# Optimization experiments

Measured on AMD Instinct MI355X. Metric: run time of the kernel, lower is better.

The kernel has to match this reference:

```python
import jax, jax.numpy as jnp
import numpy as np

GROUP_SIZE = 128
IN_FEATURES = 8192
OUT_FEATURES = 28672
TOKENS = 32


def _dequantize(qweight, qzeros, scales):
    """ExLlama q4 dequant.
    qweight: (K//8, N) int32, 8 int4 values per word packed along k.
    qzeros:  (G, N//8) int32, 8 int4 zeros per word packed along n.
    scales:  (G, N) fp16.  g = k // GROUP_SIZE; w = s * (q - (z + 1)).
    """
    shifts = jnp.arange(8, dtype=jnp.int32) * 4
    K = qweight.shape[0] * 8
    N = qweight.shape[1]
    G = qzeros.shape[0]
    # unpack weights along k: (K//8, 8, N) -> (K, N)
    q = (qweight[:, None, :] >> shifts[None, :, None]) & 15
    q = q.reshape(K, N)
    # unpack zeros along n: (G, N//8, 8) -> (G, N)
    z = (qzeros[:, :, None] >> shifts[None, None, :]) & 15
    z = z.reshape(G, N)
    # group-wise dequant: reshape k into (G, GROUP_SIZE)
    qg = q.reshape(G, GROUP_SIZE, N).astype(jnp.float16)
    zf = (z + 1).astype(jnp.float16)[:, None, :]          # ExLlama stores zero-1
    w = (qg - zf) * scales[:, None, :]                    # (G, GS, N) fp16
    return w.reshape(K, N)


def setup_inputs() -> dict:
    key = jax.random.key(0)
    k1, k2, k3, k4, k5 = jax.random.split(key, 5)
    x = jax.random.normal(k1, (TOKENS, IN_FEATURES), dtype=jnp.float16)
    qweight = jax.random.randint(k2, (IN_FEATURES // 8, OUT_FEATURES),
                                 minval=-(2**31), maxval=2**31 - 1, dtype=jnp.int32)
    qzeros = jax.random.randint(k3, (IN_FEATURES // GROUP_SIZE, OUT_FEATURES // 8),
                                minval=-(2**31), maxval=2**31 - 1, dtype=jnp.int32)
    scales = (jax.random.uniform(k4, (IN_FEATURES // GROUP_SIZE, OUT_FEATURES),
                                 dtype=jnp.float32) * 0.01 + 0.001).astype(jnp.float16)
    bias = jax.random.normal(k5, (OUT_FEATURES,), dtype=jnp.float16)
    return {"x": x, "qweight": qweight, "qzeros": qzeros,
            "scales": scales, "bias": bias}


def reference(x, qweight, qzeros, scales, bias):
    w = _dequantize(qweight, qzeros, scales)              # (K, N) fp16
    out = jnp.matmul(x.astype(jnp.float16), w)            # (T, N)
    return out + bias
```

## Files before the change

### kernel.cpp

```cpp
#include <hip/hip_runtime.h>

#define T_TOK   32
#define KDIM    8192
#define NDIM    28672
#define NGRP    64
#define NZWORDS 3584
#define NSEG    16
#define SEGK    (KDIM / NSEG)
#define GPS     (NGRP / NSEG)
#define XROW    (SEGK + 8)

typedef _Float16 half8  __attribute__((ext_vector_type(8)));
typedef _Float16 half2v __attribute__((ext_vector_type(2)));
typedef float    f32x4  __attribute__((ext_vector_type(4)));
typedef unsigned uint4v __attribute__((ext_vector_type(4)));

template<bool ATOMIC>
__global__ __launch_bounds__(256)
void exllama_gemm_deep(const int*   __restrict__ qweight,
                       const int*   __restrict__ qzeros,
                       const float* __restrict__ scales,
                       const float* __restrict__ x,
                       const float* __restrict__ bias,
                       float*       __restrict__ ws,
                       float*       __restrict__ out)
{
    __shared__ alignas(16) _Float16 xs[T_TOK * XROW];

    const int tid  = threadIdx.x;
    const int lane = tid & 63;
    const int wav  = tid >> 6;
    const int quad = lane >> 4;
    const int l16  = lane & 15;
    const int seg  = blockIdx.y;
    const int n0   = blockIdx.x * 256 + wav * 64;

    int nc[4];
    #pragma unroll
    for (int j = 0; j < 4; ++j) nc[j] = n0 + j * 16 + l16;

    const int g0 = seg * GPS;

    unsigned qw[GPS][16];
    half2v   sp[GPS][4], cp[GPS][4];
    #pragma unroll
    for (int g = 0; g < GPS; ++g) {
        const size_t rb = (size_t)((g0 + g) * 16 + quad) * NDIM;
        #pragma unroll
        for (int c = 0; c < 4; ++c)
            #pragma unroll
            for (int j = 0; j < 4; ++j)
                qw[g][c * 4 + j] = (unsigned)qweight[rb + (size_t)(c * 4) * NDIM + nc[j]];
    }
    #pragma unroll
    for (int g = 0; g < GPS; ++g) {
        #pragma unroll
        for (int j = 0; j < 4; ++j) {
            float s  = scales[(size_t)(g0 + g) * NDIM + nc[j]];
            int   zw = qzeros[(size_t)(g0 + g) * NZWORDS + (nc[j] >> 3)];
            int   z  = (zw >> ((nc[j] & 7) * 4)) & 15;
            _Float16 sh = (_Float16)s;
            _Float16 ch = (_Float16)(float)(-(1025 + z));
            sp[g][j] = (half2v){sh, sh};
            cp[g][j] = (half2v){ch, ch};
        }
    }

    {
        const int kseg0 = seg * SEGK;
        #pragma unroll
        for (int it = 0; it < (T_TOK * SEGK) / (256 * 8); ++it) {
            const int e  = it * 2048 + tid * 8;
            const int t  = e >> 9;
            const int kl = e & (SEGK - 1);
            const float* xp = x + (size_t)t * KDIM + kseg0 + kl;
            f32x4 lo = *(const f32x4*)xp;
            f32x4 hi = *(const f32x4*)(xp + 4);
            uint4v u;
            #pragma unroll
            for (int j = 0; j < 4; ++j)
                u[j] = __builtin_bit_cast(unsigned,
                          __builtin_amdgcn_cvt_pkrtz(lo[j], hi[j]));
            *(uint4v*)(xs + t * XROW + kl) = u;
        }
    }
    __syncthreads();

    f32x4 acc[4][2];
    #pragma unroll
    for (int j = 0; j < 4; ++j)
        #pragma unroll
        for (int m = 0; m < 2; ++m)
            acc[j][m] = (f32x4){0.f, 0.f, 0.f, 0.f};

    #pragma unroll
    for (int g = 0; g < GPS; ++g) {
        #pragma unroll
        for (int c = 0; c < 4; ++c) {
            const int kloc = g * 128 + c * 32 + quad * 8;
            half8 a0 = *(const half8*)(xs + l16 * XROW + kloc);
            half8 a1 = *(const half8*)(xs + (l16 + 16) * XROW + kloc);
            #pragma unroll
            for (int j = 0; j < 4; ++j) {
                const unsigned w = qw[g][c * 4 + j];
                uint4v bu;
                #pragma unroll
                for (int i = 0; i < 4; ++i) {
                    unsigned t = ((w >> (4 * i)) & 0x000F000Fu) | 0x64006400u;
                    half2v th = __builtin_bit_cast(half2v, t);
                    half2v r  = (th + cp[g][j]) * sp[g][j];
                    bu[i] = __builtin_bit_cast(unsigned, r);
                }
                half8 bf = __builtin_bit_cast(half8, bu);
                acc[j][0] = __builtin_amdgcn_mfma_f32_16x16x32_f16(a0, bf, acc[j][0], 0, 0, 0);
                acc[j][1] = __builtin_amdgcn_mfma_f32_16x16x32_f16(a1, bf, acc[j][1], 0, 0, 0);
            }
        }
    }

    if (ATOMIC) {
        #pragma unroll
        for (int j = 0; j < 4; ++j) {
            const int n  = n0 + j * 16 + l16;
            const float bb = bias[n] * (1.0f / NSEG);
            #pragma unroll
            for (int m = 0; m < 2; ++m)
                #pragma unroll
                for (int r = 0; r < 4; ++r) {
                    const int t = m * 16 + quad * 4 + r;
                    unsafeAtomicAdd(out + (size_t)t * NDIM + n, acc[j][m][r] + bb);
                }
        }
    } else {
        float* wsp = ws + (size_t)seg * (T_TOK * NDIM);
        #pragma unroll
        for (int j = 0; j < 4; ++j) {
            const int n = n0 + j * 16 + l16;
            #pragma unroll
            for (int m = 0; m < 2; ++m)
                #pragma unroll
                for (int r = 0; r < 4; ++r) {
                    const int t = m * 16 + quad * 4 + r;
                    wsp[(size_t)t * NDIM + n] = acc[j][m][r];
                }
        }
    }
}

__global__ __launch_bounds__(256)
void reduce_bias(const float* __restrict__ ws,
                 const float* __restrict__ bias,
                 float*       __restrict__ out)
{
    const int e = (blockIdx.x * 256 + threadIdx.x) * 4;
    const int n = e % NDIM;
    f32x4 sum = (f32x4){0.f, 0.f, 0.f, 0.f};
    #pragma unroll
    for (int s = 0; s < NSEG; ++s)
        sum += *(const f32x4*)(ws + (size_t)s * (T_TOK * NDIM) + e);
    f32x4 bb = *(const f32x4*)(bias + n);
    *(f32x4*)(out + e) = sum + bb;
}

extern "C" void kernel_launch(void* const* d_in, const int* in_sizes, int n_in,
                              void* d_out, int out_size, void* d_ws, size_t ws_size,
                              hipStream_t stream)
{
    const float* x  = (const float*)d_in[0];
    const int* qweight = (const int*)d_in[1];
    const int* qzeros  = (const int*)d_in[2];
    const float* sc = (const float*)d_in[3];
    const float* bs = (const float*)d_in[4];
    float* out      = (float*)d_out;

    const size_t need = (size_t)NSEG * T_TOK * NDIM * sizeof(float);
    if (ws_size >= need) {
        exllama_gemm_deep<false><<<dim3(NDIM / 256, NSEG), 256, 0, stream>>>(
            qweight, qzeros, sc, x, bs, (float*)d_ws, out);
        reduce_bias<<<(T_TOK * NDIM) / (256 * 4), 256, 0, stream>>>(
            (const float*)d_ws, bs, out);
    } else {
        exllama_gemm_deep<true><<<dim3(NDIM / 256, NSEG), 256, 0, stream>>>(
            qweight, qzeros, sc, x, bs, nullptr, out);
    }
}
```

Baseline: 200.8 us.

## Replace split-K with full-K blocks using double-buffered software pipeline

```diff
diff --git a/kernel.cpp b/kernel.cpp
--- a/kernel.cpp
+++ b/kernel.cpp
@@ -3,163 +3,139 @@
 #define T_TOK   32
 #define KDIM    8192
 #define NDIM    28672
-#define NGRP    64
-#define NZWORDS 3584
-#define NSEG    16
-#define SEGK    (KDIM / NSEG)
-#define GPS     (NGRP / NSEG)
-#define XROW    (SEGK + 8)
+#define NZW     3584
+#define PHK     256
+#define NPH     (KDIM / PHK)
+#define GPP     (PHK / 128)
+#define XROW    (PHK + 8)
+#define XIT     ((T_TOK * PHK) / (256 * 8))
 
 typedef _Float16 half8  __attribute__((ext_vector_type(8)));
 typedef _Float16 half2v __attribute__((ext_vector_type(2)));
 typedef float    f32x4  __attribute__((ext_vector_type(4)));
 typedef unsigned uint4v __attribute__((ext_vector_type(4)));
 
-template<bool ATOMIC>
 __global__ __launch_bounds__(256)
-void exllama_gemm_deep(const int*   __restrict__ qweight,
-                       const int*   __restrict__ qzeros,
-                       const float* __restrict__ scales,
-                       const float* __restrict__ x,
-                       const float* __restrict__ bias,
-                       float*       __restrict__ ws,
-                       float*       __restrict__ out)
+void exllama_gemm_fullk(const int*   __restrict__ qweight,
+                        const int*   __restrict__ qzeros,
+                        const float* __restrict__ scales,
+                        const float* __restrict__ x,
+                        const float* __restrict__ bias,
+                        float*       __restrict__ out)
 {
-    __shared__ alignas(16) _Float16 xs[T_TOK * XROW];
+    __shared__ alignas(16) _Float16 xs[2][T_TOK * XROW];
 
     const int tid  = threadIdx.x;
     const int lane = tid & 63;
     const int wav  = tid >> 6;
     const int quad = lane >> 4;
     const int l16  = lane & 15;
-    const int seg  = blockIdx.y;
-    const int n0   = blockIdx.x * 256 + wav * 64;
+    const int n    = blockIdx.x * 64 + wav * 16 + l16;
 
-    int nc[4];
+    const float* xbase[XIT];
+    int          lofs[XIT];
     #pragma unroll
-    for (int j = 0; j < 4; ++j) nc[j] = n0 + j * 16 + l16;
-
-    const int g0 = seg * GPS;
-
-    unsigned qw[GPS][16];
-    half2v   sp[GPS][4], cp[GPS][4];
-    #pragma unroll
-    for (int g = 0; g < GPS; ++g) {
-        const size_t rb = (size_t)((g0 + g) * 16 + quad) * NDIM;
-        #pragma unroll
-        for (int c = 0; c < 4; ++c)
-            #pragma unroll
-            for (int j = 0; j < 4; ++j)
-                qw[g][c * 4 + j] = (unsigned)qweight[rb + (size_t)(c * 4) * NDIM + nc[j]];
-    }
-    #pragma unroll
-    for (int g = 0; g < GPS; ++g) {
-        #pragma unroll
-        for (int j = 0; j < 4; ++j) {
-            float s  = scales[(size_t)(g0 + g) * NDIM + nc[j]];
-            int   zw = qzeros[(size_t)(g0 + g) * NZWORDS + (nc[j] >> 3)];
-            int   z  = (zw >> ((nc[j] & 7) * 4)) & 15;
-            _Float16 sh = (_Float16)s;
-            _Float16 ch = (_Float16)(float)(-(1025 + z));
-            sp[g][j] = (half2v){sh, sh};
-            cp[g][j] = (half2v){ch, ch};
-        }
+    for (int it = 0; it < XIT; ++it) {
+        const int e  = it * 2048 + tid * 8;
+        const int t  = e >> 8;
+        const int kl = e & (PHK - 1);
+        xbase[it] = x + (size_t)t * KDIM + kl;
+        lofs[it]  = t * XROW + kl;
     }
 
-    {
-        const int kseg0 = seg * SEGK;
+    f32x4 xlo[XIT], xhi[XIT];
+    auto LOADX = [&](int p) {
         #pragma unroll
-        for (int it = 0; it < (T_TOK * SEGK) / (256 * 8); ++it) {
-            const int e  = it * 2048 + tid * 8;
-            const int t  = e >> 9;
-            const int kl = e & (SEGK - 1);
-            const float* xp = x + (size_t)t * KDIM + kseg0 + kl;
-            f32x4 lo = *(const f32x4*)xp;
-            f32x4 hi = *(const f32x4*)(xp + 4);
+        for (int it = 0; it < XIT; ++it) {
+            const float* xp = xbase[it] + p * PHK;
+            xlo[it] = *(const f32x4*)xp;
+            xhi[it] = *(const f32x4*)(xp + 4);
+        }
+    };
+    auto CVTW = [&](_Float16* buf) {
+        #pragma unroll
+        for (int it = 0; it < XIT; ++it) {
             uint4v u;
             #pragma unroll
             for (int j = 0; j < 4; ++j)
                 u[j] = __builtin_bit_cast(unsigned,
-                          __builtin_amdgcn_cvt_pkrtz(lo[j], hi[j]));
-            *(uint4v*)(xs + t * XROW + kl) = u;
+                          __builtin_amdgcn_cvt_pkrtz(xlo[it][j], xhi[it][j]));
+            *(uint4v*)(buf + lofs[it]) = u;
         }
-    }
-    __syncthreads();
+    };
+    auto LOADQ = [&](unsigned* qw, half2v* sp, half2v* cp, int p) {
+        #pragma unroll
+        for (int g = 0; g < GPP; ++g) {
+            const size_t rb = (size_t)(p * (PHK / 8) + g * 16 + quad) * NDIM + n;
+            #pragma unroll
+            for (int c = 0; c < 4; ++c)
+                qw[g * 4 + c] = (unsigned)qweight[rb + (size_t)(c * 4) * NDIM];
+            const float s  = scales[(size_t)(p * GPP + g) * NDIM + n];
+            const int   zw = qzeros[(size_t)(p * GPP + g) * NZW + (n >> 3)];
+            const int   z  = (zw >> ((n & 7) * 4)) & 15;
+            const _Float16 sh = (_Float16)s;
+            const _Float16 ch = (_Float16)(float)(-(1025 + z));
+            sp[g] = (half2v){sh, sh};
+            cp[g] = (half2v){ch, ch};
+        }
+    };
 
-    f32x4 acc[4][2];
-    #pragma unroll
-    for (int j = 0; j < 4; ++j)
+    f32x4 acc0 = (f32x4){0.f, 0.f, 0.f, 0.f};
+    f32x4 acc1 = (f32x4){0.f, 0.f, 0.f, 0.f};
+    auto COMPUTE = [&](const unsigned* qw, const half2v* sp, const half2v* cp,
+                       const _Float16* buf) {
         #pragma unroll
-        for (int m = 0; m < 2; ++m)
-            acc[j][m] = (f32x4){0.f, 0.f, 0.f, 0.f};
-
-    #pragma unroll
-    for (int g = 0; g < GPS; ++g) {
-        #pragma unroll
-        for (int c = 0; c < 4; ++c) {
-            const int kloc = g * 128 + c * 32 + quad * 8;
-            half8 a0 = *(const half8*)(xs + l16 * XROW + kloc);
-            half8 a1 = *(const half8*)(xs + (l16 + 16) * XROW + kloc);
+        for (int g = 0; g < GPP; ++g) {
             #pragma unroll
-            for (int j = 0; j < 4; ++j) {
-                const unsigned w = qw[g][c * 4 + j];
+            for (int c = 0; c < 4; ++c) {
+                const int kloc = g * 128 + c * 32 + quad * 8;
+                half8 a0 = *(const half8*)(buf + l16 * XROW + kloc);
+                half8 a1 = *(const half8*)(buf + (l16 + 16) * XROW + kloc);
+                const unsigned w = qw[g * 4 + c];
                 uint4v bu;
                 #pragma unroll
                 for (int i = 0; i < 4; ++i) {
                     unsigned t = ((w >> (4 * i)) & 0x000F000Fu) | 0x64006400u;
                     half2v th = __builtin_bit_cast(half2v, t);
-                    half2v r  = (th + cp[g][j]) * sp[g][j];
+                    half2v r  = (th + cp[g]) * sp[g];
                     bu[i] = __builtin_bit_cast(unsigned, r);
                 }
                 half8 bf = __builtin_bit_cast(half8, bu);
-                acc[j][0] = __builtin_amdgcn_mfma_f32_16x16x32_f16(a0, bf, acc[j][0], 0, 0, 0);
-                acc[j][1] = __builtin_amdgcn_mfma_f32_16x16x32_f16(a1, bf, acc[j][1], 0, 0, 0);
+                acc0 = __builtin_amdgcn_mfma_f32_16x16x32_f16(a0, bf, acc0, 0, 0, 0);
+                acc1 = __builtin_amdgcn_mfma_f32_16x16x32_f16(a1, bf, acc1, 0, 0, 0);
             }
         }
+    };
+
+    unsigned qwA[4 * GPP], qwB[4 * GPP];
+    half2v   spA[GPP], cpA[GPP], spB[GPP], cpB[GPP];
+
+    LOADX(0);
+    LOADQ(qwA, spA, cpA, 0);
+    CVTW(xs[0]);
+    __syncthreads();
+
+    for (int pp = 0; pp < NPH; pp += 2) {
+        LOADX(pp + 1);
+        LOADQ(qwB, spB, cpB, pp + 1);
+        COMPUTE(qwA, spA, cpA, xs[0]);
+        CVTW(xs[1]);
+        __syncthreads();
+        if (pp + 2 < NPH) {
+            LOADX(pp + 2);
+            LOADQ(qwA, spA, cpA, pp + 2);
+        }
+        COMPUTE(qwB, spB, cpB, xs[1]);
+        if (pp + 2 < NPH) CVTW(xs[0]);
+        __syncthreads();
     }
 
-    if (ATOMIC) {
-        #pragma unroll
-        for (int j = 0; j < 4; ++j) {
-            const int n  = n0 + j * 16 + l16;
-            const float bb = bias[n] * (1.0f / NSEG);
-            #pragma unroll
-            for (int m = 0; m < 2; ++m)
-                #pragma unroll
-                for (int r = 0; r < 4; ++r) {
-                    const int t = m * 16 + quad * 4 + r;
-                    unsafeAtomicAdd(out + (size_t)t * NDIM + n, acc[j][m][r] + bb);
-                }
-        }
-    } else {
-        float* wsp = ws + (size_t)seg * (T_TOK * NDIM);
-        #pragma unroll
-        for (int j = 0; j < 4; ++j) {
-            const int n = n0 + j * 16 + l16;
-            #pragma unroll
-            for (int m = 0; m < 2; ++m)
-                #pragma unroll
-                for (int r = 0; r < 4; ++r) {
-                    const int t = m * 16 + quad * 4 + r;
-                    wsp[(size_t)t * NDIM + n] = acc[j][m][r];
-                }
-        }
+    const float bb = bias[n];
+    #pragma unroll
+    for (int r = 0; r < 4; ++r) {
+        out[(size_t)(quad * 4 + r) * NDIM + n]        = acc0[r] + bb;
+        out[(size_t)(16 + quad * 4 + r) * NDIM + n]   = acc1[r] + bb;
     }
-}
-
-__global__ __launch_bounds__(256)
-void reduce_bias(const float* __restrict__ ws,
-                 const float* __restrict__ bias,
-                 float*       __restrict__ out)
-{
-    const int e = (blockIdx.x * 256 + threadIdx.x) * 4;
-    const int n = e % NDIM;
-    f32x4 sum = (f32x4){0.f, 0.f, 0.f, 0.f};
-    #pragma unroll
-    for (int s = 0; s < NSEG; ++s)
-        sum += *(const f32x4*)(ws + (size_t)s * (T_TOK * NDIM) + e);
-    f32x4 bb = *(const f32x4*)(bias + n);
-    *(f32x4*)(out + e) = sum + bb;
 }
 
 extern "C" void kernel_launch(void* const* d_in, const int* in_sizes, int n_in,
@@ -173,14 +149,7 @@
     const float* bs = (const float*)d_in[4];
     float* out      = (float*)d_out;
 
-    const size_t need = (size_t)NSEG * T_TOK * NDIM * sizeof(float);
-    if (ws_size >= need) {
-        exllama_gemm_deep<false><<<dim3(NDIM / 256, NSEG), 256, 0, stream>>>(
-            qweight, qzeros, sc, x, bs, (float*)d_ws, out);
-        reduce_bias<<<(T_TOK * NDIM) / (256 * 4), 256, 0, stream>>>(
-            (const float*)d_ws, bs, out);
-    } else {
-        exllama_gemm_deep<true><<<dim3(NDIM / 256, NSEG), 256, 0, stream>>>(
-            qweight, qzeros, sc, x, bs, nullptr, out);
-    }
+    (void)d_ws; (void)ws_size;
+    exllama_gemm_fullk<<<dim3(NDIM / 64), 256, 0, stream>>>(
+        qweight, qzeros, sc, x, bs, out);
 }
```

Measured after the change: 211.0 us. 5.1% more time.
